# Kernel tuning notes

Measured on AMD Instinct MI355X. Metric: run time of the kernel, lower is better.

## Reference

```python
import itertools
import jax, jax.numpy as jnp
import numpy as np

B, S, D = 512, 49, 448
H, KD, RATIO, RES = 8, 32, 4, 7
EKD = KD * RATIO              # expanded key dim = 128
QKV_OUT = H * (2 * KD + EKD)  # 1536
MLP_HID = D * 4               # 1792
EPS = 1e-5
LS_INIT = 1e-5


def _build_bias_idxs():
    points = list(itertools.product(range(RES), range(RES)))
    offsets = {}
    idxs = []
    for p1 in points:
        for p2 in points:
            off = (abs(p1[0] - p2[0]), abs(p1[1] - p2[1]))
            if off not in offsets:
                offsets[off] = len(offsets)
            idxs.append(offsets[off])
    return np.asarray(idxs, dtype=np.int32).reshape(len(points), len(points)), len(offsets)


def setup_inputs() -> dict:
    key = jax.random.key(0)
    ks = jax.random.split(key, 10)
    idxs_np, n_off = _build_bias_idxs()  # (49,49), 49 unique offsets
    std = 0.02
    return {
        "hidden_states": jax.random.normal(ks[0], (B, S, D), jnp.float32),
        "ln1_g": jnp.ones((D,), jnp.float32),
        "ln1_b": jnp.zeros((D,), jnp.float32),
        "qkv_w": jax.random.normal(ks[1], (D, QKV_OUT), jnp.float32) * std,
        "qkv_b": jnp.zeros((QKV_OUT,), jnp.float32),
        "attention_biases": jax.random.normal(ks[2], (H, n_off), jnp.float32) * std,
        "proj_w": jax.random.normal(ks[3], (H * EKD, D), jnp.float32) * std,
        "proj_b": jnp.zeros((D,), jnp.float32),
        "ln2_g": jnp.ones((D,), jnp.float32),
        "ln2_b": jnp.zeros((D,), jnp.float32),
        "mlp_w1": jax.random.normal(ks[4], (D, MLP_HID), jnp.float32) * std,
        "mlp_b1": jnp.zeros((MLP_HID,), jnp.float32),
        "mlp_w2": jax.random.normal(ks[5], (MLP_HID, D), jnp.float32) * std,
        "mlp_b2": jnp.zeros((D,), jnp.float32),
        "ls1": jnp.full((D,), LS_INIT, jnp.float32),
        "ls2": jnp.full((D,), LS_INIT, jnp.float32),
        "attention_bias_idxs": jnp.asarray(idxs_np),
    }


def _layernorm(x, g, b):
    mu = jnp.mean(x, axis=-1, keepdims=True)
    var = jnp.mean(jnp.square(x - mu), axis=-1, keepdims=True)
    return (x - mu) * jax.lax.rsqrt(var + EPS) * g + b


def reference(hidden_states, ln1_g, ln1_b, qkv_w, qkv_b, attention_biases,
              proj_w, proj_b, ln2_g, ln2_b, mlp_w1, mlp_b1, mlp_w2, mlp_b2,
              ls1, ls2, attention_bias_idxs):
    x = hidden_states
    # --- token mixer (self-attention with relative-position bias) ---
    h = _layernorm(x, ln1_g, ln1_b)
    qkv = h @ qkv_w + qkv_b                           # [B,S,1536]
    qkv = qkv.reshape(B, S, H, 2 * KD + EKD)
    q, k, v = jnp.split(qkv, [KD, 2 * KD], axis=3)    # [B,S,H,32/32/128]
    scale = KD ** (-0.5)
    scores = jnp.einsum("bqhd,bkhd->bhqk", q, k) * scale
    bias = attention_biases[:, attention_bias_idxs]   # [H,S,S]
    probs = jax.nn.softmax(scores + bias[None], axis=-1)
    ctx = jnp.einsum("bhqk,bkhd->bqhd", probs, v).reshape(B, S, H * EKD)
    attn_out = ctx @ proj_w + proj_b                  # [B,S,D]
    # --- residual with layerscale (drop_path = identity in eval) ---
    x = x + ls1 * attn_out
    # --- MLP branch ---
    h2 = _layernorm(x, ln2_g, ln2_b)
    m = jax.nn.gelu(h2 @ mlp_w1 + mlp_b1, approximate=False)
    m = m @ mlp_w2 + mlp_b2
    x = x + ls2 * m
    return x
```

## Files before the change

kernel.cpp:

```cpp
#include <hip/hip_runtime.h>
#include <hip/hip_bf16.h>

#define BB 512
#define SS 49
#define DD 448
#define HH 8
#define QKVO 1536
#define MLPH 1792
#define MM (BB*SS)

using bf16_t = __hip_bfloat16;
typedef __attribute__((ext_vector_type(8))) short short8;
typedef __attribute__((ext_vector_type(4))) float f32x4;

__device__ __forceinline__ void gload_lds16(const void* g, void* l) {
  __builtin_amdgcn_global_load_lds(
      (const __attribute__((address_space(1))) void*)g,
      (__attribute__((address_space(3))) void*)l,
      16, 0, 0);
}

__global__ void prep_kernel(const float* __restrict__ qkv_w, const float* __restrict__ proj_w,
                            const float* __restrict__ w1, const float* __restrict__ w2,
                            const float* __restrict__ ab, const int* __restrict__ idxs,
                            bf16_t* __restrict__ qkv_wT, bf16_t* __restrict__ proj_wT,
                            bf16_t* __restrict__ w1T, bf16_t* __restrict__ w2T,
                            bf16_t* __restrict__ bias_pad)
{
  int idx = blockIdx.x * 256 + threadIdx.x;
  if (idx < 688128) {
    int n = idx / 448, k = idx % 448;
    qkv_wT[idx] = __float2bfloat16(qkv_w[k*1536 + n]);
  } else if ((idx -= 688128) < 458752) {
    int n = idx / 1024, k = idx % 1024;
    proj_wT[idx] = __float2bfloat16(proj_w[k*448 + n]);
  } else if ((idx -= 458752) < 802816) {
    int n = idx / 448, k = idx % 448;
    w1T[idx] = __float2bfloat16(w1[k*1792 + n]);
  } else if ((idx -= 802816) < 802816) {
    int n = idx / 1792, k = idx % 1792;
    w2T[idx] = __float2bfloat16(w2[k*448 + n]);
  } else if ((idx -= 802816) < 32768) {
    int h = idx >> 12, r = (idx >> 6) & 63, c = idx & 63;
    float v = (r < SS && c < SS) ? ab[h*49 + idxs[r*49 + c]] : -1e30f;
    bias_pad[idx] = __float2bfloat16(v);
  }
}

__global__ __launch_bounds__(256) void ln_kernel(const float* __restrict__ x,
                                                 const float* __restrict__ g,
                                                 const float* __restrict__ b,
                                                 bf16_t* __restrict__ out)
{
  const int w = threadIdx.x >> 6, lane = threadIdx.x & 63;
  const int row = blockIdx.x * 4 + w;
  const float* xr = x + (size_t)row * DD;
  float v[7];
  float s = 0.f;
#pragma unroll
  for (int j = 0; j < 7; ++j) { v[j] = xr[lane + 64*j]; s += v[j]; }
#pragma unroll
  for (int off = 32; off; off >>= 1) s += __shfl_xor(s, off, 64);
  const float mu = s * (1.0f/448.0f);
  float q = 0.f;
#pragma unroll
  for (int j = 0; j < 7; ++j) { float d = v[j] - mu; q += d*d; }
#pragma unroll
  for (int off = 32; off; off >>= 1) q += __shfl_xor(q, off, 64);
  const float rstd = rsqrtf(q * (1.0f/448.0f) + 1e-5f);
  bf16_t* orow = out + (size_t)row * DD;
#pragma unroll
  for (int j = 0; j < 7; ++j) {
    int c = lane + 64*j;
    orow[c] = __float2bfloat16((v[j] - mu) * rstd * g[c] + b[c]);
  }
}

enum { EP_BF16 = 0, EP_RES1 = 1, EP_GELU = 2, EP_RES2 = 3 };

template<int EPI>
__global__ __launch_bounds__(256, 2) void gemm_bf16(
    const bf16_t* __restrict__ A, const bf16_t* __restrict__ Bt,
    const float* __restrict__ bias, const float* __restrict__ resid,
    const float* __restrict__ ls, bf16_t* __restrict__ Obf,
    float* __restrict__ Of, int N, int K)
{
  __shared__ __align__(16) char lds[32768];
  const int t = threadIdx.x;
  const int lane = t & 63;
  const int w = t >> 6;
  const int m0 = blockIdx.x * 128;
  const int n0 = blockIdx.y * 128;
  const int fr = lane & 15;
  const int fq = lane >> 4;
  const int wm = (w >> 1) * 64;
  const int wn = (w & 1) * 64;

  f32x4 acc[4][4];
#pragma unroll
  for (int i = 0; i < 4; ++i)
#pragma unroll
    for (int j = 0; j < 4; ++j)
      acc[i][j] = f32x4{0.f, 0.f, 0.f, 0.f};

  const int rsub = t >> 3;
  const int g8 = (t & 7) ^ (rsub & 7);
  const int wbase = (t & 192) * 16;
  const int nkt = K >> 6;

  for (int kt = 0; kt < nkt; ++kt) {
    const int k0 = kt << 6;
#pragma unroll
    for (int i = 0; i < 4; ++i) {
      const int ra = i*32 + rsub;
      gload_lds16(A + (size_t)(m0 + ra) * K + (k0 + g8*8), lds + i*4096 + wbase);
      int rb = n0 + i*32 + rsub;
      if (rb >= N) rb = N - 1;
      gload_lds16(Bt + (size_t)rb * K + (k0 + g8*8), lds + 16384 + i*4096 + wbase);
    }
    __syncthreads();
#pragma unroll
    for (int kk = 0; kk < 2; ++kk) {
      short8 af[4], bfr[4];
#pragma unroll
      for (int i = 0; i < 4; ++i) {
        const int ra = wm + i*16 + fr;
        const int ca = (fq + kk*4) ^ (ra & 7);
        af[i] = *(const short8*)(lds + ra*128 + ca*16);
        const int rb2 = wn + i*16 + fr;
        const int cb = (fq + kk*4) ^ (rb2 & 7);
        bfr[i] = *(const short8*)(lds + 16384 + rb2*128 + cb*16);
      }
#pragma unroll
      for (int mi = 0; mi < 4; ++mi)
#pragma unroll
        for (int ni = 0; ni < 4; ++ni)
          acc[mi][ni] = __builtin_amdgcn_mfma_f32_16x16x32_bf16(af[mi], bfr[ni], acc[mi][ni], 0, 0, 0);
    }
    __syncthreads();
  }

#pragma unroll
  for (int mi = 0; mi < 4; ++mi) {
#pragma unroll
    for (int ni = 0; ni < 4; ++ni) {
      const int col = n0 + wn + ni*16 + fr;
      if (col < N) {
        const float bc = bias[col];
        const int row0 = m0 + wm + mi*16 + fq*4;
#pragma unroll
        for (int ri = 0; ri < 4; ++ri) {
          const size_t o = (size_t)(row0 + ri) * N + col;
          const float v = acc[mi][ni][ri] + bc;
          if constexpr (EPI == EP_BF16) {
            Obf[o] = __float2bfloat16(v);
          } else if constexpr (EPI == EP_GELU) {
            Obf[o] = __float2bfloat16(0.5f * v * (1.0f + erff(v * 0.7071067811865475f)));
          } else if constexpr (EPI == EP_RES1) {
            Of[o] = resid[o] + ls[col] * v;
          } else {
            Of[o] = Of[o] + ls[col] * v;
          }
        }
      }
    }
  }
}

__global__ __launch_bounds__(64) void attn_mfma_kernel(const bf16_t* __restrict__ qkv,
                                                       const bf16_t* __restrict__ bias_pad,
                                                       bf16_t* __restrict__ ctx)
{
  __shared__ __align__(16) bf16_t VsF[64*128];
  __shared__ __align__(16) bf16_t PsF[64*72];
  const int b = blockIdx.x >> 3, h = blockIdx.x & 7;
  const int l = threadIdx.x;
  const int fr = l & 15, g = l >> 4;
  const size_t base = ((size_t)b * SS) * QKVO + (size_t)h * 192;

  for (int c = l; c < 1024; c += 64) {
    const int j = c >> 4, ch = c & 15;
    const int jc = j < SS ? j : SS - 1;
    short8 v = *(const short8*)(qkv + base + (size_t)jc * QKVO + 64 + ch*8);
    *(short8*)(&VsF[j*128 + ((ch ^ (j >> 3)) & 15)*8]) = v;
  }

  short8 qf[4], kf[4];
#pragma unroll
  for (int mi = 0; mi < 4; ++mi) {
    int qr = mi*16 + fr; if (qr > SS-1) qr = SS-1;
    qf[mi] = *(const short8*)(qkv + base + (size_t)qr * QKVO + g*8);
    int kr = mi*16 + fr; if (kr > SS-1) kr = SS-1;
    kf[mi] = *(const short8*)(qkv + base + (size_t)kr * QKVO + 32 + g*8);
  }
  f32x4 sc[4][4];
#pragma unroll
  for (int mi = 0; mi < 4; ++mi)
#pragma unroll
    for (int ni = 0; ni < 4; ++ni)
      sc[mi][ni] = f32x4{0.f,0.f,0.f,0.f};
#pragma unroll
  for (int mi = 0; mi < 4; ++mi)
#pragma unroll
    for (int ni = 0; ni < 4; ++ni)
      sc[mi][ni] = __builtin_amdgcn_mfma_f32_16x16x32_bf16(qf[mi], kf[ni], sc[mi][ni], 0, 0, 0);

  const float scale = 0.17677669529663687f;
  const bf16_t* bp = bias_pad + (size_t)h * 4096;
#pragma unroll
  for (int mi = 0; mi < 4; ++mi) {
#pragma unroll
    for (int ri = 0; ri < 4; ++ri) {
      const int r = mi*16 + g*4 + ri;
      float v0 = sc[mi][0][ri]*scale + __bfloat162float(bp[r*64 +      fr]);
      float v1 = sc[mi][1][ri]*scale + __bfloat162float(bp[r*64 + 16 + fr]);
      float v2 = sc[mi][2][ri]*scale + __bfloat162float(bp[r*64 + 32 + fr]);
      float v3 = sc[mi][3][ri]*scale + __bfloat162float(bp[r*64 + 48 + fr]);
      float m = fmaxf(fmaxf(v0, v1), fmaxf(v2, v3));
#pragma unroll
      for (int off = 8; off; off >>= 1) m = fmaxf(m, __shfl_xor(m, off, 64));
      v0 = __expf(v0 - m); v1 = __expf(v1 - m);
      v2 = __expf(v2 - m); v3 = __expf(v3 - m);
      float s = v0 + v1 + v2 + v3;
#pragma unroll
      for (int off = 8; off; off >>= 1) s += __shfl_xor(s, off, 64);
      const float inv = 1.0f / s;
      PsF[r*72 +      fr] = __float2bfloat16(v0 * inv);
      PsF[r*72 + 16 + fr] = __float2bfloat16(v1 * inv);
      PsF[r*72 + 32 + fr] = __float2bfloat16(v2 * inv);
      PsF[r*72 + 48 + fr] = __float2bfloat16(v3 * inv);
    }
  }
  __syncthreads();

  short8 pf[4][2];
#pragma unroll
  for (int mi = 0; mi < 4; ++mi)
#pragma unroll
    for (int ks = 0; ks < 2; ++ks)
      pf[mi][ks] = *(const short8*)(&PsF[(mi*16 + fr)*72 + ks*32 + g*8]);

#pragma unroll
  for (int ni = 0; ni < 8; ++ni) {
    const int e = ni*16 + fr;
    short8 vf[2];
#pragma unroll
    for (int ks = 0; ks < 2; ++ks) {
      const int jb = ks*32 + g*8;
#pragma unroll
      for (int jj = 0; jj < 8; ++jj) {
        const int j = jb + jj;
        const int ch = ((e >> 3) ^ (j >> 3)) & 15;
        vf[ks][jj] = *(const short*)(&VsF[j*128 + ch*8 + (e & 7)]);
      }
    }
    f32x4 acc2[4];
#pragma unroll
    for (int mi = 0; mi < 4; ++mi) acc2[mi] = f32x4{0.f,0.f,0.f,0.f};
#pragma unroll
    for (int ks = 0; ks < 2; ++ks)
#pragma unroll
      for (int mi = 0; mi < 4; ++mi)
        acc2[mi] = __builtin_amdgcn_mfma_f32_16x16x32_bf16(pf[mi][ks], vf[ks], acc2[mi], 0, 0, 0);
#pragma unroll
    for (int mi = 0; mi < 4; ++mi) {
#pragma unroll
      for (int ri = 0; ri < 4; ++ri) {
        const int q = mi*16 + g*4 + ri;
        if (q < SS)
          ctx[((size_t)b * SS + q) * 1024 + h*128 + e] = __float2bfloat16(acc2[mi][ri]);
      }
    }
  }
}

extern "C" void kernel_launch(void* const* d_in, const int* in_sizes, int n_in,
                              void* d_out, int out_size, void* d_ws, size_t ws_size,
                              hipStream_t stream) {
  const float* x      = (const float*)d_in[0];
  const float* ln1_g  = (const float*)d_in[1];
  const float* ln1_b  = (const float*)d_in[2];
  const float* qkv_w  = (const float*)d_in[3];
  const float* qkv_b  = (const float*)d_in[4];
  const float* ab     = (const float*)d_in[5];
  const float* proj_w = (const float*)d_in[6];
  const float* proj_b = (const float*)d_in[7];
  const float* ln2_g  = (const float*)d_in[8];
  const float* ln2_b  = (const float*)d_in[9];
  const float* w1     = (const float*)d_in[10];
  const float* b1     = (const float*)d_in[11];
  const float* w2     = (const float*)d_in[12];
  const float* b2     = (const float*)d_in[13];
  const float* ls1    = (const float*)d_in[14];
  const float* ls2    = (const float*)d_in[15];
  const int*   idxs   = (const int*)d_in[16];
  float* out = (float*)d_out;
  char* ws = (char*)d_ws;

  bf16_t* h_buf    = (bf16_t*)(ws);
  bf16_t* qkv_buf  = (bf16_t*)(ws + 22478848);
  bf16_t* ctx_buf  = (bf16_t*)(ws + 99549184);
  bf16_t* m_buf    = (bf16_t*)(ws + 22478848);
  bf16_t* qkv_wT   = (bf16_t*)(ws + 150929408);
  bf16_t* proj_wT  = (bf16_t*)(ws + 152305664);
  bf16_t* w1T      = (bf16_t*)(ws + 153223168);
  bf16_t* w2T      = (bf16_t*)(ws + 154828800);
  bf16_t* bias_pad = (bf16_t*)(ws + 156434432);

  const int prep_total = 688128 + 458752 + 802816 + 802816 + 32768;
  prep_kernel<<<(prep_total + 255)/256, 256, 0, stream>>>(
      qkv_w, proj_w, w1, w2, ab, idxs, qkv_wT, proj_wT, w1T, w2T, bias_pad);

  ln_kernel<<<MM/4, 256, 0, stream>>>(x, ln1_g, ln1_b, h_buf);

  gemm_bf16<EP_BF16><<<dim3(MM/128, 12), 256, 0, stream>>>(
      h_buf, qkv_wT, qkv_b, nullptr, nullptr, qkv_buf, nullptr, QKVO, DD);

  attn_mfma_kernel<<<BB*HH, 64, 0, stream>>>(qkv_buf, bias_pad, ctx_buf);

  gemm_bf16<EP_RES1><<<dim3(MM/128, 4), 256, 0, stream>>>(
      ctx_buf, proj_wT, proj_b, x, ls1, nullptr, out, DD, 1024);

  ln_kernel<<<MM/4, 256, 0, stream>>>(out, ln2_g, ln2_b, h_buf);

  gemm_bf16<EP_GELU><<<dim3(MM/128, 14), 256, 0, stream>>>(
      h_buf, w1T, b1, nullptr, nullptr, m_buf, nullptr, MLPH, DD);

  gemm_bf16<EP_RES2><<<dim3(MM/128, 4), 256, 0, stream>>>(
      m_buf, w2T, b2, nullptr, ls2, nullptr, out, DD, MLPH);
}
```

Baseline: 342.9 us.

## Split-K the N=448 GEMMs, fuse reductions with residual/LN2, swizzle block order

The two narrow GEMMs (proj and MLP-down, N=448) now run split-K by two and write bf16 partial sums. New reduction kernels add the partials, bias, layerscale and residual, and the first of them also performs LayerNorm2. The GEMM grid becomes 1-D with an XCD-aware block swizzle, and global load pointers are precomputed. This gives more blocks on the narrow GEMMs and keeps tiles that share operands together, at the cost of extra bf16 partial traffic, two extra launches, and bf16 rounding of the partials.

After: 324.8 us. -5.3%, faster.

```diff
diff --git a/kernel.cpp b/kernel.cpp
--- a/kernel.cpp
+++ b/kernel.cpp
@@ -76,21 +76,85 @@
   }
 }
 
-enum { EP_BF16 = 0, EP_RES1 = 1, EP_GELU = 2, EP_RES2 = 3 };
-
-template<int EPI>
-__global__ __launch_bounds__(256, 2) void gemm_bf16(
+__global__ __launch_bounds__(256) void red1_ln2_kernel(
+    const float* __restrict__ x, const bf16_t* __restrict__ p0,
+    const bf16_t* __restrict__ p1, const float* __restrict__ pb,
+    const float* __restrict__ ls1, const float* __restrict__ g,
+    const float* __restrict__ b, float* __restrict__ out, bf16_t* __restrict__ h2)
+{
+  const int w = threadIdx.x >> 6, lane = threadIdx.x & 63;
+  const int row = blockIdx.x * 4 + w;
+  const float* xr = x + (size_t)row * DD;
+  const bf16_t* p0r = p0 + (size_t)row * DD;
+  const bf16_t* p1r = p1 + (size_t)row * DD;
+  float* orow = out + (size_t)row * DD;
+  float v[7];
+  float s = 0.f;
+#pragma unroll
+  for (int j = 0; j < 7; ++j) {
+    const int c = lane + 64*j;
+    const float pv = __bfloat162float(p0r[c]) + __bfloat162float(p1r[c]) + pb[c];
+    v[j] = xr[c] + ls1[c] * pv;
+    orow[c] = v[j];
+    s += v[j];
+  }
+#pragma unroll
+  for (int off = 32; off; off >>= 1) s += __shfl_xor(s, off, 64);
+  const float mu = s * (1.0f/448.0f);
+  float q = 0.f;
+#pragma unroll
+  for (int j = 0; j < 7; ++j) { float d = v[j] - mu; q += d*d; }
+#pragma unroll
+  for (int off = 32; off; off >>= 1) q += __shfl_xor(q, off, 64);
+  const float rstd = rsqrtf(q * (1.0f/448.0f) + 1e-5f);
+  bf16_t* hrow = h2 + (size_t)row * DD;
+#pragma unroll
+  for (int j = 0; j < 7; ++j) {
+    const int c = lane + 64*j;
+    hrow[c] = __float2bfloat16((v[j] - mu) * rstd * g[c] + b[c]);
+  }
+}
+
+__global__ __launch_bounds__(256) void red2_kernel(
+    const bf16_t* __restrict__ q0, const bf16_t* __restrict__ q1,
+    const float* __restrict__ pb, const float* __restrict__ ls2,
+    float* __restrict__ out)
+{
+  const int w = threadIdx.x >> 6, lane = threadIdx.x & 63;
+  const int row = blockIdx.x * 4 + w;
+  const bf16_t* q0r = q0 + (size_t)row * DD;
+  const bf16_t* q1r = q1 + (size_t)row * DD;
+  float* orow = out + (size_t)row * DD;
+#pragma unroll
+  for (int j = 0; j < 7; ++j) {
+    const int c = lane + 64*j;
+    const float pv = __bfloat162float(q0r[c]) + __bfloat162float(q1r[c]) + pb[c];
+    orow[c] = orow[c] + ls2[c] * pv;
+  }
+}
+
+enum { EP_BF16 = 0, EP_GELU = 2, EP_PART = 4 };
+
+template<int EPI, int NSPLIT>
+__global__ __launch_bounds__(256, 2) void gemmr_bf16(
     const bf16_t* __restrict__ A, const bf16_t* __restrict__ Bt,
-    const float* __restrict__ bias, const float* __restrict__ resid,
-    const float* __restrict__ ls, bf16_t* __restrict__ Obf,
-    float* __restrict__ Of, int N, int K)
+    const float* __restrict__ bias, bf16_t* __restrict__ O0,
+    bf16_t* __restrict__ O1, int N, int K, int gy)
 {
   __shared__ __align__(16) char lds[32768];
   const int t = threadIdx.x;
   const int lane = t & 63;
   const int w = t >> 6;
-  const int m0 = blockIdx.x * 128;
-  const int n0 = blockIdx.y * 128;
+
+  const int chunk = gridDim.x >> 3;
+  const int swz = (blockIdx.x & 7) * chunk + (blockIdx.x >> 3);
+  const int m0 = (swz / (gy * NSPLIT)) * 128;
+  const int rr = swz % (gy * NSPLIT);
+  const int n0 = (rr / NSPLIT) * 128;
+  const int sp = rr % NSPLIT;
+  const int ksub = K / NSPLIT;
+  const int kbase = sp * ksub;
+
   const int fr = lane & 15;
   const int fq = lane >> 4;
   const int wm = (w >> 1) * 64;
@@ -105,18 +169,25 @@
 
   const int rsub = t >> 3;
   const int g8 = (t & 7) ^ (rsub & 7);
-  const int wbase = (t & 192) * 16;
-  const int nkt = K >> 6;
+  const int wbase = w * 1024;
+  const int nkt = ksub >> 6;
+
+  const bf16_t* gA[4];
+  const bf16_t* gB[4];
+#pragma unroll
+  for (int i = 0; i < 4; ++i) {
+    gA[i] = A + (size_t)(m0 + i*32 + rsub) * K + kbase + g8*8;
+    int rb = n0 + i*32 + rsub;
+    if (rb >= N) rb = N - 1;
+    gB[i] = Bt + (size_t)rb * K + kbase + g8*8;
+  }
 
   for (int kt = 0; kt < nkt; ++kt) {
-    const int k0 = kt << 6;
+    const int ko = kt << 6;
 #pragma unroll
     for (int i = 0; i < 4; ++i) {
-      const int ra = i*32 + rsub;
-      gload_lds16(A + (size_t)(m0 + ra) * K + (k0 + g8*8), lds + i*4096 + wbase);
-      int rb = n0 + i*32 + rsub;
-      if (rb >= N) rb = N - 1;
-      gload_lds16(Bt + (size_t)rb * K + (k0 + g8*8), lds + 16384 + i*4096 + wbase);
+      gload_lds16(gA[i] + ko, lds + i*4096 + wbase);
+      gload_lds16(gB[i] + ko, lds + 16384 + i*4096 + wbase);
     }
     __syncthreads();
 #pragma unroll
@@ -140,26 +211,24 @@
     __syncthreads();
   }
 
+  bf16_t* P = (NSPLIT == 2 && sp == 1) ? O1 : O0;
 #pragma unroll
   for (int mi = 0; mi < 4; ++mi) {
 #pragma unroll
     for (int ni = 0; ni < 4; ++ni) {
       const int col = n0 + wn + ni*16 + fr;
       if (col < N) {
-        const float bc = bias[col];
+        float bc = 0.f;
+        if constexpr (EPI != EP_PART) bc = bias[col];
         const int row0 = m0 + wm + mi*16 + fq*4;
 #pragma unroll
         for (int ri = 0; ri < 4; ++ri) {
           const size_t o = (size_t)(row0 + ri) * N + col;
           const float v = acc[mi][ni][ri] + bc;
-          if constexpr (EPI == EP_BF16) {
-            Obf[o] = __float2bfloat16(v);
-          } else if constexpr (EPI == EP_GELU) {
-            Obf[o] = __float2bfloat16(0.5f * v * (1.0f + erff(v * 0.7071067811865475f)));
-          } else if constexpr (EPI == EP_RES1) {
-            Of[o] = resid[o] + ls[col] * v;
+          if constexpr (EPI == EP_GELU) {
+            P[o] = __float2bfloat16(0.5f * v * (1.0f + erff(v * 0.7071067811865475f)));
           } else {
-            Of[o] = Of[o] + ls[col] * v;
+            P[o] = __float2bfloat16(v);
           }
         }
       }
@@ -301,6 +370,10 @@
   bf16_t* qkv_buf  = (bf16_t*)(ws + 22478848);
   bf16_t* ctx_buf  = (bf16_t*)(ws + 99549184);
   bf16_t* m_buf    = (bf16_t*)(ws + 22478848);
+  bf16_t* p0       = (bf16_t*)(ws + 22478848);
+  bf16_t* p1       = (bf16_t*)(ws + 44957696);
+  bf16_t* q0       = (bf16_t*)(ws);
+  bf16_t* q1       = (bf16_t*)(ws + 112394240);
   bf16_t* qkv_wT   = (bf16_t*)(ws + 150929408);
   bf16_t* proj_wT  = (bf16_t*)(ws + 152305664);
   bf16_t* w1T      = (bf16_t*)(ws + 153223168);
@@ -313,19 +386,22 @@
 
   ln_kernel<<<MM/4, 256, 0, stream>>>(x, ln1_g, ln1_b, h_buf);
 
-  gemm_bf16<EP_BF16><<<dim3(MM/128, 12), 256, 0, stream>>>(
-      h_buf, qkv_wT, qkv_b, nullptr, nullptr, qkv_buf, nullptr, QKVO, DD);
+  gemmr_bf16<EP_BF16, 1><<<196*12, 256, 0, stream>>>(
+      h_buf, qkv_wT, qkv_b, qkv_buf, nullptr, QKVO, DD, 12);
 
   attn_mfma_kernel<<<BB*HH, 64, 0, stream>>>(qkv_buf, bias_pad, ctx_buf);
 
-  gemm_bf16<EP_RES1><<<dim3(MM/128, 4), 256, 0, stream>>>(
-      ctx_buf, proj_wT, proj_b, x, ls1, nullptr, out, DD, 1024);
-
-  ln_kernel<<<MM/4, 256, 0, stream>>>(out, ln2_g, ln2_b, h_buf);
-
-  gemm_bf16<EP_GELU><<<dim3(MM/128, 14), 256, 0, stream>>>(
-      h_buf, w1T, b1, nullptr, nullptr, m_buf, nullptr, MLPH, DD);
-
-  gemm_bf16<EP_RES2><<<dim3(MM/128, 4), 256, 0, stream>>>(
-      m_buf, w2T, b2, nullptr, ls2, nullptr, out, DD, MLPH);
-}
+  gemmr_bf16<EP_PART, 2><<<196*4*2, 256, 0, stream>>>(
+      ctx_buf, proj_wT, nullptr, p0, p1, DD, 1024, 4);
+
+  red1_ln2_kernel<<<MM/4, 256, 0, stream>>>(
+      x, p0, p1, proj_b, ls1, ln2_g, ln2_b, out, h_buf);
+
+  gemmr_bf16<EP_GELU, 1><<<196*14, 256, 0, stream>>>(
+      h_buf, w1T, b1, m_buf, nullptr, MLPH, DD, 14);
+
+  gemmr_bf16<EP_PART, 2><<<196*4*2, 256, 0, stream>>>(
+      m_buf, w2T, nullptr, q0, q1, DD, MLPH, 4);
+
+  red2_kernel<<<MM/4, 256, 0, stream>>>(q0, q1, b2, ls2, out);
+}
```
